# Kernel optimization log

Hardware: AMD Instinct MI355X
Metric: run time of the kernel (lower is better)

Reference implementation:

```python
import jax, jax.numpy as jnp
import numpy as np

LENGTHS = [1024, 768, 896, 512, 1024, 640, 1024, 768, 512, 896, 1024, 704]  # sum = 9792
EMBED, HEADS = 1024, 16
HDIM = EMBED // HEADS  # 64
ROPE_BASE = 10000.0


def _rotate_half(x):
    half = x.shape[-1] // 2
    return jnp.concatenate([-x[..., half:], x[..., :half]], axis=-1)


def setup_inputs() -> dict:
    key = jax.random.key(0)
    ks = jax.random.split(key, 8)
    T = sum(LENGTHS)
    hidden = jax.random.normal(ks[0], (T, EMBED), jnp.float32)
    # RoPE cos/sin: positions restart at 0 within each packed segment
    pos = np.concatenate([np.arange(l) for l in LENGTHS]).astype(np.float32)  # [T]
    inv_freq = 1.0 / (ROPE_BASE ** (np.arange(0, HDIM, 2, dtype=np.float32) / HDIM))
    freqs = np.outer(pos, inv_freq)                       # [T, HDIM//2]
    emb = np.concatenate([freqs, freqs], axis=-1)         # [T, HDIM]
    cos = jnp.asarray(np.cos(emb), jnp.float32)
    sin = jnp.asarray(np.sin(emb), jnp.float32)
    s = 0.02
    q_w = jax.random.normal(ks[1], (EMBED, EMBED), jnp.float32) * s
    k_w = jax.random.normal(ks[2], (EMBED, EMBED), jnp.float32) * s
    v_w = jax.random.normal(ks[3], (EMBED, EMBED), jnp.float32) * s
    out_w = jax.random.normal(ks[4], (EMBED, EMBED), jnp.float32) * s
    q_b = jax.random.normal(ks[5], (EMBED,), jnp.float32) * s
    v_b = jax.random.normal(ks[6], (EMBED,), jnp.float32) * s
    out_b = jax.random.normal(ks[7], (EMBED,), jnp.float32) * s
    return {
        "hidden_states": hidden, "cos": cos, "sin": sin,
        "q_w": q_w, "q_b": q_b, "k_w": k_w, "v_w": v_w, "v_b": v_b,
        "out_w": out_w, "out_b": out_b,
        "seq_len": jnp.array(LENGTHS, jnp.int32),
        "max_seqlen": 1024,
    }


def reference(hidden_states, cos, sin, q_w, q_b, k_w, v_w, v_b, out_w, out_b,
              seq_len, max_seqlen):
    T, D = hidden_states.shape
    H, Dh = HEADS, D // HEADS
    B = seq_len.shape[0]
    L = max_seqlen  # static python int

    # Projections (torch Linear: y = x @ W.T + b; k_proj has no bias)
    q = (hidden_states @ q_w.T + q_b).reshape(T, H, Dh)
    k = (hidden_states @ k_w.T).reshape(T, H, Dh)
    v = (hidden_states @ v_w.T + v_b).reshape(T, H, Dh)

    # Inline RoPE (cos/sin broadcast over heads)
    c = cos[:, None, :]
    s = sin[:, None, :]
    q = q * c + _rotate_half(q) * s
    k = k * c + _rotate_half(k) * s

    # Gather packed tokens into padded [B, L, H, Dh] (honors ragged structure:
    # no [T, T] dense score matrix, only per-segment [L, L] blocks)
    cu = jnp.concatenate([jnp.zeros((1,), seq_len.dtype), jnp.cumsum(seq_len)])[:-1]  # [B] starts
    ar = jnp.arange(L)
    idx = cu[:, None] + ar[None, :]                 # [B, L] token ids
    valid = ar[None, :] < seq_len[:, None]          # [B, L]
    idxc = jnp.minimum(idx, T - 1)
    qp = q[idxc]                                    # [B, L, H, Dh]
    kp = k[idxc]
    vp = v[idxc]

    scale = 1.0 / jnp.sqrt(jnp.float32(Dh))
    scores = jnp.einsum('blhd,bmhd->bhlm', qp, kp) * scale  # [B, H, L, L]
    causal = ar[:, None] >= ar[None, :]             # [L, L]
    mask = valid[:, None, None, :] & causal[None, None, :, :]
    scores = jnp.where(mask, scores, jnp.float32(-1e30))
    probs = jax.nn.softmax(scores, axis=-1)
    attn = jnp.einsum('bhlm,bmhd->blhd', probs, vp).reshape(B, L, D)

    # Scatter valid tokens back to packed layout [T, D]
    attn = attn * valid[..., None].astype(attn.dtype)
    flat = jnp.zeros((T, D), attn.dtype).at[idxc.reshape(-1)].add(attn.reshape(-1, D))
    return flat @ out_w.T + out_b
```

## Files before the change

### kernel.cpp

```cpp
#include <hip/hip_runtime.h>

typedef __bf16 bf16;
typedef __bf16 bf16x8 __attribute__((ext_vector_type(8)));
typedef __bf16 bf16x4 __attribute__((ext_vector_type(4)));
typedef float  f32x4  __attribute__((ext_vector_type(4)));

#define T_TOTAL 9792
#define EMBED   1024
#define NHEAD   16
#define HDIM    64

__constant__ int c_seq_start[12] = {0,1024,1792,2688,3200,4224,4864,5888,6656,7168,8064,9088};
__constant__ int c_tiles_cum[13] = {0,16,28,42,50,66,76,92,104,112,126,142,153};

typedef __attribute__((address_space(1))) unsigned int gu32;
typedef __attribute__((address_space(3))) unsigned int lu32;

__device__ __forceinline__ void load_lds16(const void* g, void* l) {
    __builtin_amdgcn_global_load_lds((gu32*)g, (lu32*)l, 16, 0, 0);
}

__device__ __forceinline__ f32x4 mfma16(bf16x8 a, bf16x8 b, f32x4 c) {
    return __builtin_amdgcn_mfma_f32_16x16x32_bf16(a, b, c, 0, 0, 0);
}

struct CvtArgs {
    const void* src[10];
    bf16*       dst[10];
    int         n[10];
    int         cum[10];
};

__global__ void to_bf16_fused(CvtArgs a, const unsigned short* __restrict__ disc)
{
    const bool f32 = (disc[0] == 0);
    const int blk = blockIdx.x;
    int seg = 0;
    #pragma unroll
    for (int i = 1; i < 10; ++i) if (blk >= a.cum[i]) seg = i;
    int i0 = (blk - a.cum[seg]) * 2048 + threadIdx.x * 8;
    if (i0 >= a.n[seg]) return;
    bf16x8 o;
    if (f32) {
        const float4* s = (const float4*)((const float*)a.src[seg] + i0);
        float4 x = s[0], y = s[1];
        o[0]=(bf16)x.x; o[1]=(bf16)x.y; o[2]=(bf16)x.z; o[3]=(bf16)x.w;
        o[4]=(bf16)y.x; o[5]=(bf16)y.y; o[6]=(bf16)y.z; o[7]=(bf16)y.w;
    } else {
        o = *(const bf16x8*)((const bf16*)a.src[seg] + i0);
    }
    *(bf16x8*)(a.dst[seg] + i0) = o;
}

__device__ __forceinline__ void map_block2(int L, int NX, int NY, int& x, int& y)
{
    const int per = 8 * NY;
    const int nfull = NX >> 3;
    const int full = nfull * per;
    if (L < full) { int sc = L / per, rem = L % per; x = sc * 8 + (rem & 7); y = rem >> 3; }
    else {
        int rem = L - full;
        int tw = NX - nfull * 8;
        x = nfull * 8 + rem % tw; y = rem / tw;
    }
}

__device__ __forceinline__
void gemm_core256(const bf16* __restrict__ A, const bf16* __restrict__ W,
                  int M, int m0, int n0, f32x4 (&acc)[8][4],
                  bf16* lA, bf16* lB)
{
    const int tid  = threadIdx.x;
    const int wave = tid >> 6, lane = tid & 63;
    const int lrow = lane >> 3;
    const int gsw  = (lane & 7) ^ lrow;
    const int ln   = lane & 15, lq = lane >> 4;
    const int e7   = ln & 7;
    const int wm   = (wave >> 2) & 1;
    const int wn   = wave & 3;

    auto stage = [&](int kt, int buf) {
        const int k0 = kt * 64;
        bf16* dA = lA + buf * (256 * 64);
        bf16* dB = lB + buf * (256 * 64);
        #pragma unroll
        for (int j = 0; j < 4; ++j) {
            int r = j * 64 + wave * 8;
            int gr = m0 + r + lrow; if (gr > M - 1) gr = M - 1;
            load_lds16(A + (size_t)gr * EMBED + k0 + gsw * 8, dA + r * 64);
            load_lds16(W + (size_t)(n0 + r + lrow) * EMBED + k0 + gsw * 8, dB + r * 64);
        }
    };

    stage(0, 0);
    __syncthreads();

    for (int kt = 0; kt < 16; ++kt) {
        const int p = kt & 1;
        const bf16* sA = lA + p * (256 * 64);
        const bf16* sB = lB + p * (256 * 64);
        #pragma unroll
        for (int ph = 0; ph < 4; ++ph) {
            const int mh = ph >> 1, nh = ph & 1;
            if (ph == 0 && kt + 1 < 16) stage(kt + 1, p ^ 1);

            bf16x8 af[2][4], bfr[2][2];
            #pragma unroll
            for (int kb = 0; kb < 2; ++kb) {
                #pragma unroll
                for (int mi = 0; mi < 4; ++mi)
                    af[kb][mi] = *(const bf16x8*)
                        &sA[(wm * 128 + mh * 64 + mi * 16 + ln) * 64 + (((kb * 4 + lq) ^ e7) * 8)];
                #pragma unroll
                for (int niq = 0; niq < 2; ++niq)
                    bfr[kb][niq] = *(const bf16x8*)
                        &sB[(wn * 64 + nh * 32 + niq * 16 + ln) * 64 + (((kb * 4 + lq) ^ e7) * 8)];
            }
            __builtin_amdgcn_s_barrier();
            asm volatile("s_waitcnt lgkmcnt(0)" ::: "memory");
            __builtin_amdgcn_s_setprio(1);
            #pragma unroll
            for (int kb = 0; kb < 2; ++kb)
                #pragma unroll
                for (int mi = 0; mi < 4; ++mi)
                    #pragma unroll
                    for (int niq = 0; niq < 2; ++niq)
                        acc[mh * 4 + mi][nh * 2 + niq] =
                            mfma16(af[kb][mi], bfr[kb][niq], acc[mh * 4 + mi][nh * 2 + niq]);
            __builtin_amdgcn_s_setprio(0);
            if (ph == 3 && kt + 1 < 16)
                asm volatile("s_waitcnt vmcnt(0)" ::: "memory");
            __builtin_amdgcn_s_barrier();
        }
    }
}

__global__ __launch_bounds__(512, 2)
void gemm_qkv(const bf16* __restrict__ A,
              const bf16* __restrict__ Wq, const bf16* __restrict__ Wk,
              const bf16* __restrict__ Wv, const bf16* __restrict__ qb,
              const bf16* __restrict__ vb,
              const bf16* __restrict__ cosb, const bf16* __restrict__ sinb,
              bf16* __restrict__ Cq, bf16* __restrict__ Ck,
              bf16* __restrict__ Vt, int M)
{
    __shared__ __align__(16) bf16 lA[2 * 256 * 64];
    __shared__ __align__(16) bf16 lB[2 * 256 * 64];

    int x, yy;
    map_block2(blockIdx.x, 39, 12, x, yy);
    const int which = yy >> 2;
    const int m0 = x * 256, n0 = (yy & 3) * 256;

    const bf16* W = (which == 0) ? Wq : (which == 1) ? Wk : Wv;
    f32x4 acc[8][4] = {};
    gemm_core256(A, W, M, m0, n0, acc, lA, lB);

    const int tid  = threadIdx.x;
    const int wave = tid >> 6, lane = tid & 63;
    const int ln   = lane & 15, lq = lane >> 4;
    const int wm   = (wave >> 2) & 1, wn = wave & 3;
    const int rbase = m0 + wm * 128;
    const int cbase = n0 + wn * 64;

    if (which < 2) {
        bf16* C = (which == 0) ? Cq : Ck;
        const bf16* bias = (which == 0) ? qb : nullptr;
        #pragma unroll
        for (int mi = 0; mi < 8; ++mi) {
            int trow = rbase + mi * 16 + lq * 4;
            if (trow >= M) continue;
            #pragma unroll
            for (int ni = 0; ni < 2; ++ni) {
                int d    = ni * 16 + ln;
                int col0 = cbase + d;
                int col1 = col0 + 32;
                float b0 = bias ? (float)bias[col0] : 0.0f;
                float b1 = bias ? (float)bias[col1] : 0.0f;
                #pragma unroll
                for (int r = 0; r < 4; ++r) {
                    int t = trow + r;
                    float c = (float)cosb[t * HDIM + d];
                    float s = (float)sinb[t * HDIM + d];
                    float x0 = acc[mi][ni][r] + b0;
                    float x1 = acc[mi][ni + 2][r] + b1;
                    C[(size_t)t * EMBED + col0] = (bf16)(x0 * c - x1 * s);
                    C[(size_t)t * EMBED + col1] = (bf16)(x1 * c + x0 * s);
                }
            }
        }
    } else {
        #pragma unroll
        for (int mi = 0; mi < 8; ++mi) {
            int trow = rbase + mi * 16 + lq * 4;
            if (trow >= M) continue;
            #pragma unroll
            for (int ni = 0; ni < 4; ++ni) {
                int d = ni * 16 + ln;
                float bv = (float)vb[cbase + d];
                bf16x4 o;
                #pragma unroll
                for (int r = 0; r < 4; ++r) o[r] = (bf16)(acc[mi][ni][r] + bv);
                *(bf16x4*)&Vt[(size_t)(cbase + d) * T_TOTAL + trow] = o;
            }
        }
    }
}

__global__ __launch_bounds__(512, 2)
void gemm_out(const bf16* __restrict__ A, const bf16* __restrict__ W,
              const bf16* __restrict__ bias, void* __restrict__ out, int M,
              const unsigned short* __restrict__ disc)
{
    __shared__ __align__(16) bf16 lA[2 * 256 * 64];
    __shared__ __align__(16) bf16 lB[2 * 256 * 64];

    int x, yy;
    map_block2(blockIdx.x, 39, 4, x, yy);
    const int m0 = x * 256, n0 = yy * 256;

    f32x4 acc[8][4] = {};
    gemm_core256(A, W, M, m0, n0, acc, lA, lB);

    const bool f32 = (disc[0] == 0);
    const int tid  = threadIdx.x;
    const int wave = tid >> 6, lane = tid & 63;
    const int ln   = lane & 15, lq = lane >> 4;
    const int wm   = (wave >> 2) & 1, wn = wave & 3;
    const int rbase = m0 + wm * 128;
    const int cbase = n0 + wn * 64;

    #pragma unroll
    for (int mi = 0; mi < 8; ++mi) {
        int trow = rbase + mi * 16 + lq * 4;
        if (trow >= M) continue;
        #pragma unroll
        for (int ni = 0; ni < 4; ++ni) {
            int col = cbase + ni * 16 + ln;
            float bv = (float)bias[col];
            #pragma unroll
            for (int r = 0; r < 4; ++r) {
                float v = acc[mi][ni][r] + bv;
                size_t idx = (size_t)(trow + r) * EMBED + col;
                if (f32) ((float*)out)[idx] = v;
                else     ((bf16*)out)[idx]  = (bf16)v;
            }
        }
    }
}

__global__ __launch_bounds__(256, 3)
void attn_kernel(const bf16* __restrict__ Q, const bf16* __restrict__ K,
                 const bf16* __restrict__ Vt, bf16* __restrict__ O)
{
    __shared__ __align__(16) bf16 sK[2][64 * 64];
    __shared__ __align__(16) bf16 sV[2][64 * 64];
    __shared__ __align__(16) bf16 sQP[4 * 16 * 72];

    const int tid  = threadIdx.x;
    const int wave = tid >> 6, lane = tid & 63;
    const int lrow = lane >> 3;
    const int gsw  = (lane & 7) ^ lrow;
    const int ln   = lane & 15, lq = lane >> 4;
    const int e7   = ln & 7;
    const int h = blockIdx.y;

    int b = 0;
    #pragma unroll
    for (int i = 1; i < 13; ++i) if ((int)blockIdx.x >= c_tiles_cum[i]) b = i;
    const int qt = blockIdx.x - c_tiles_cum[b];
    const int t0 = c_seq_start[b] + qt * 64;
    const int kvb0 = c_seq_start[b];

    for (int p = 0; p < 2; ++p) {
        int r = p * 32 + wave * 8;
        load_lds16(Q  + (size_t)(t0 + r + lrow) * EMBED + h * HDIM + gsw * 8, &sQP[r * 64]);
        load_lds16(K  + (size_t)(kvb0 + r + lrow) * EMBED + h * HDIM + gsw * 8, &sK[0][r * 64]);
        load_lds16(Vt + (size_t)(h * HDIM + r + lrow) * T_TOTAL + kvb0 + gsw * 8, &sV[0][r * 64]);
    }

    bf16x8 qf[2];
    f32x4 oacc[4] = {};
    float m_i = -1e30f, l_i = 0.0f;
    const float sc = 0.125f * 1.44269504088896f;
    const int q_loc = wave * 16 + ln;
    bf16* sP = &sQP[wave * 16 * 72];

    for (int j = 0; j <= qt; ++j) {
        __syncthreads();
        const int cur = j & 1;
        if (j == 0) {
            qf[0] = *(const bf16x8*)&sQP[q_loc * 64 + ((0 + lq) ^ e7) * 8];
            qf[1] = *(const bf16x8*)&sQP[q_loc * 64 + ((4 + lq) ^ e7) * 8];
            __syncthreads();
        }
        if (j < qt) {
            const int kvb = kvb0 + (j + 1) * 64;
            const int nxt = cur ^ 1;
            for (int p = 0; p < 2; ++p) {
                int r = p * 32 + wave * 8;
                load_lds16(K  + (size_t)(kvb + r + lrow) * EMBED + h * HDIM + gsw * 8, &sK[nxt][r * 64]);
                load_lds16(Vt + (size_t)(h * HDIM + r + lrow) * T_TOTAL + kvb + gsw * 8, &sV[nxt][r * 64]);
            }
        }

        f32x4 s[4] = {};
        #pragma unroll
        for (int kk = 0; kk < 2; ++kk)
            #pragma unroll
            for (int ni = 0; ni < 4; ++ni) {
                bf16x8 kf = *(const bf16x8*)&sK[cur][(ni * 16 + ln) * 64 + (((kk * 4 + lq) ^ e7) * 8)];
                s[ni] = mfma16(kf, qf[kk], s[ni]);
            }

        float pb[4][4];
        if (j == qt) {
            #pragma unroll
            for (int ni = 0; ni < 4; ++ni)
                #pragma unroll
                for (int r = 0; r < 4; ++r) {
                    int kv = ni * 16 + lq * 4 + r;
                    pb[ni][r] = (kv <= q_loc) ? s[ni][r] * sc : -1e30f;
                }
        } else {
            #pragma unroll
            for (int ni = 0; ni < 4; ++ni)
                #pragma unroll
                for (int r = 0; r < 4; ++r)
                    pb[ni][r] = s[ni][r] * sc;
        }

        float mx = pb[0][0];
        #pragma unroll
        for (int ni = 0; ni < 4; ++ni)
            #pragma unroll
            for (int r = 0; r < 4; ++r) mx = fmaxf(mx, pb[ni][r]);
        mx = fmaxf(mx, __shfl_xor(mx, 16));
        mx = fmaxf(mx, __shfl_xor(mx, 32));
        float mnew  = fmaxf(m_i, mx);
        float alpha = exp2f(m_i - mnew);
        m_i = mnew;

        float rs = 0.0f;
        #pragma unroll
        for (int ni = 0; ni < 4; ++ni)
            #pragma unroll
            for (int r = 0; r < 4; ++r) {
                float pe = exp2f(pb[ni][r] - mnew);
                pb[ni][r] = pe;
                rs += pe;
            }
        rs += __shfl_xor(rs, 16);
        rs += __shfl_xor(rs, 32);
        l_i = l_i * alpha + rs;
        #pragma unroll
        for (int d = 0; d < 4; ++d)
            #pragma unroll
            for (int r = 0; r < 4; ++r) oacc[d][r] *= alpha;

        #pragma unroll
        for (int ni = 0; ni < 4; ++ni) {
            bf16x4 w4;
            #pragma unroll
            for (int r = 0; r < 4; ++r) w4[r] = (bf16)pb[ni][r];
            *(bf16x4*)&sP[ln * 72 + ni * 16 + lq * 4] = w4;
        }
        asm volatile("s_waitcnt lgkmcnt(0)" ::: "memory");

        #pragma unroll
        for (int kk = 0; kk < 2; ++kk) {
            bf16x8 pf = *(const bf16x8*)&sP[ln * 72 + kk * 32 + lq * 8];
            #pragma unroll
            for (int d = 0; d < 4; ++d) {
                bf16x8 vf = *(const bf16x8*)&sV[cur][(d * 16 + ln) * 64 + (((kk * 4 + lq) ^ e7) * 8)];
                oacc[d] = mfma16(vf, pf, oacc[d]);
            }
        }
    }

    const float inv = 1.0f / l_i;
    const size_t row = (size_t)(t0 + q_loc) * EMBED + h * HDIM;
    #pragma unroll
    for (int d = 0; d < 4; ++d) {
        bf16x4 o4;
        #pragma unroll
        for (int r = 0; r < 4; ++r) o4[r] = (bf16)(oacc[d][r] * inv);
        *(bf16x4*)&O[row + d * 16 + lq * 4] = o4;
    }
}

extern "C" void kernel_launch(void* const* d_in, const int* in_sizes, int n_in,
                              void* d_out, int out_size, void* d_ws, size_t ws_size,
                              hipStream_t stream)
{
    const unsigned short* disc = (const unsigned short*)d_in[1];

    const size_t SZ  = (size_t)T_TOTAL * EMBED;
    const size_t CS  = (size_t)T_TOTAL * HDIM;
    const size_t WSZ = (size_t)EMBED * EMBED;

    bf16* p = (bf16*)d_ws;
    bf16* ch   = p; p += SZ;
    bf16* ccos = p; p += CS;
    bf16* csin = p; p += CS;
    bf16* cqw  = p; p += WSZ;
    bf16* ckw  = p; p += WSZ;
    bf16* cvw  = p; p += WSZ;
    bf16* cow  = p; p += WSZ;
    bf16* cqb  = p; p += EMBED;
    bf16* cvb  = p; p += EMBED;
    bf16* cob  = p; p += EMBED;
    bf16* wq   = p; p += SZ;
    bf16* wk   = p; p += SZ;
    bf16* wvt  = p; p += SZ;

    CvtArgs ca;
    const void* srcs[10] = {d_in[0], d_in[1], d_in[2], d_in[3], d_in[5],
                            d_in[6], d_in[8], d_in[4], d_in[7], d_in[9]};
    bf16* dsts[10] = {ch, ccos, csin, cqw, ckw, cvw, cow, cqb, cvb, cob};
    int   ns[10]   = {(int)SZ, (int)CS, (int)CS, (int)WSZ, (int)WSZ,
                      (int)WSZ, (int)WSZ, EMBED, EMBED, EMBED};
    int cum = 0;
    for (int i = 0; i < 10; ++i) {
        ca.src[i] = srcs[i]; ca.dst[i] = dsts[i]; ca.n[i] = ns[i];
        ca.cum[i] = cum;
        cum += (ns[i] + 2047) / 2048;
    }
    to_bf16_fused<<<cum, 256, 0, stream>>>(ca, disc);

    gemm_qkv<<<39 * 12, 512, 0, stream>>>(ch, cqw, ckw, cvw, cqb, cvb,
                                          ccos, csin, wq, wk, wvt, T_TOTAL);
    attn_kernel<<<dim3(153, 16), 256, 0, stream>>>(wq, wk, wvt, wq);
    gemm_out<<<39 * 4, 512, 0, stream>>>(wq, cow, cob, d_out, T_TOTAL, disc);
}
```

Before: 331.4 us.

## Replace GEMM double buffer with a 4-stage K=32 LDS ring pipeline

```diff
diff --git a/kernel.cpp b/kernel.cpp
--- a/kernel.cpp
+++ b/kernel.cpp
@@ -67,71 +67,63 @@
 
 __device__ __forceinline__
 void gemm_core256(const bf16* __restrict__ A, const bf16* __restrict__ W,
-                  int M, int m0, int n0, f32x4 (&acc)[8][4],
-                  bf16* lA, bf16* lB)
+                  int M, int m0, int n0, f32x4 (&acc)[8][4], bf16* lds)
 {
     const int tid  = threadIdx.x;
     const int wave = tid >> 6, lane = tid & 63;
-    const int lrow = lane >> 3;
-    const int gsw  = (lane & 7) ^ lrow;
     const int ln   = lane & 15, lq = lane >> 4;
-    const int e7   = ln & 7;
     const int wm   = (wave >> 2) & 1;
     const int wn   = wave & 3;
 
-    auto stage = [&](int kt, int buf) {
-        const int k0 = kt * 64;
-        bf16* dA = lA + buf * (256 * 64);
-        bf16* dB = lB + buf * (256 * 64);
-        #pragma unroll
-        for (int j = 0; j < 4; ++j) {
-            int r = j * 64 + wave * 8;
-            int gr = m0 + r + lrow; if (gr > M - 1) gr = M - 1;
-            load_lds16(A + (size_t)gr * EMBED + k0 + gsw * 8, dA + r * 64);
-            load_lds16(W + (size_t)(n0 + r + lrow) * EMBED + k0 + gsw * 8, dB + r * 64);
-        }
+    const int srow = tid >> 2;
+    const int sg   = (tid & 3) * 8;
+
+    int r0 = m0 + srow;        if (r0 > M - 1) r0 = M - 1;
+    int r1 = m0 + 128 + srow;  if (r1 > M - 1) r1 = M - 1;
+    const bf16* gA0 = A + (size_t)r0 * EMBED + sg;
+    const bf16* gA1 = A + (size_t)r1 * EMBED + sg;
+    const bf16* gB0 = W + (size_t)(n0 + srow) * EMBED + sg;
+    const bf16* gB1 = W + (size_t)(n0 + 128 + srow) * EMBED + sg;
+
+    auto stage = [&](int t) {
+        const int k0 = t * 32;
+        bf16* dA = lds + (t & 3) * 16384;
+        bf16* dB = dA + 8192;
+        load_lds16(gA0 + k0, dA + tid * 8);
+        load_lds16(gA1 + k0, dA + 4096 + tid * 8);
+        load_lds16(gB0 + k0, dB + tid * 8);
+        load_lds16(gB1 + k0, dB + 4096 + tid * 8);
     };
 
-    stage(0, 0);
-    __syncthreads();
-
-    for (int kt = 0; kt < 16; ++kt) {
-        const int p = kt & 1;
-        const bf16* sA = lA + p * (256 * 64);
-        const bf16* sB = lB + p * (256 * 64);
-        #pragma unroll
-        for (int ph = 0; ph < 4; ++ph) {
-            const int mh = ph >> 1, nh = ph & 1;
-            if (ph == 0 && kt + 1 < 16) stage(kt + 1, p ^ 1);
-
-            bf16x8 af[2][4], bfr[2][2];
-            #pragma unroll
-            for (int kb = 0; kb < 2; ++kb) {
-                #pragma unroll
-                for (int mi = 0; mi < 4; ++mi)
-                    af[kb][mi] = *(const bf16x8*)
-                        &sA[(wm * 128 + mh * 64 + mi * 16 + ln) * 64 + (((kb * 4 + lq) ^ e7) * 8)];
-                #pragma unroll
-                for (int niq = 0; niq < 2; ++niq)
-                    bfr[kb][niq] = *(const bf16x8*)
-                        &sB[(wn * 64 + nh * 32 + niq * 16 + ln) * 64 + (((kb * 4 + lq) ^ e7) * 8)];
-            }
-            __builtin_amdgcn_s_barrier();
-            asm volatile("s_waitcnt lgkmcnt(0)" ::: "memory");
-            __builtin_amdgcn_s_setprio(1);
-            #pragma unroll
-            for (int kb = 0; kb < 2; ++kb)
-                #pragma unroll
-                for (int mi = 0; mi < 4; ++mi)
-                    #pragma unroll
-                    for (int niq = 0; niq < 2; ++niq)
-                        acc[mh * 4 + mi][nh * 2 + niq] =
-                            mfma16(af[kb][mi], bfr[kb][niq], acc[mh * 4 + mi][nh * 2 + niq]);
-            __builtin_amdgcn_s_setprio(0);
-            if (ph == 3 && kt + 1 < 16)
-                asm volatile("s_waitcnt vmcnt(0)" ::: "memory");
-            __builtin_amdgcn_s_barrier();
-        }
+    stage(0); stage(1); stage(2);
+
+    const int aoff = (wm * 128 + ln) * 32 + lq * 8;
+    const int boff = (wn * 64  + ln) * 32 + lq * 8;
+
+    for (int t = 0; t < 32; ++t) {
+        if (t < 30)       asm volatile("s_waitcnt vmcnt(8)" ::: "memory");
+        else if (t == 30) asm volatile("s_waitcnt vmcnt(4)" ::: "memory");
+        else              asm volatile("s_waitcnt vmcnt(0)" ::: "memory");
+        __builtin_amdgcn_s_barrier();
+        if (t + 3 < 32) stage(t + 3);
+
+        const bf16* sA = lds + (t & 3) * 16384;
+        const bf16* sB = sA + 8192;
+        bf16x8 af[8], bfr[4];
+        #pragma unroll
+        for (int mi = 0; mi < 8; ++mi)
+            af[mi] = *(const bf16x8*)&sA[aoff + mi * 512];
+        #pragma unroll
+        for (int ni = 0; ni < 4; ++ni)
+            bfr[ni] = *(const bf16x8*)&sB[boff + ni * 512];
+
+        __builtin_amdgcn_s_setprio(1);
+        #pragma unroll
+        for (int mi = 0; mi < 8; ++mi)
+            #pragma unroll
+            for (int ni = 0; ni < 4; ++ni)
+                acc[mi][ni] = mfma16(af[mi], bfr[ni], acc[mi][ni]);
+        __builtin_amdgcn_s_setprio(0);
     }
 }
 
@@ -144,8 +136,7 @@
               bf16* __restrict__ Cq, bf16* __restrict__ Ck,
               bf16* __restrict__ Vt, int M)
 {
-    __shared__ __align__(16) bf16 lA[2 * 256 * 64];
-    __shared__ __align__(16) bf16 lB[2 * 256 * 64];
+    __shared__ __align__(16) bf16 lds[4 * 16384];
 
     int x, yy;
     map_block2(blockIdx.x, 39, 12, x, yy);
@@ -154,7 +145,7 @@
 
     const bf16* W = (which == 0) ? Wq : (which == 1) ? Wk : Wv;
     f32x4 acc[8][4] = {};
-    gemm_core256(A, W, M, m0, n0, acc, lA, lB);
+    gemm_core256(A, W, M, m0, n0, acc, lds);
 
     const int tid  = threadIdx.x;
     const int wave = tid >> 6, lane = tid & 63;
@@ -212,15 +203,14 @@
               const bf16* __restrict__ bias, void* __restrict__ out, int M,
               const unsigned short* __restrict__ disc)
 {
-    __shared__ __align__(16) bf16 lA[2 * 256 * 64];
-    __shared__ __align__(16) bf16 lB[2 * 256 * 64];
+    __shared__ __align__(16) bf16 lds[4 * 16384];
 
     int x, yy;
     map_block2(blockIdx.x, 39, 4, x, yy);
     const int m0 = x * 256, n0 = yy * 256;
 
     f32x4 acc[8][4] = {};
-    gemm_core256(A, W, M, m0, n0, acc, lA, lB);
+    gemm_core256(A, W, M, m0, n0, acc, lds);
 
     const bool f32 = (disc[0] == 0);
     const int tid  = threadIdx.x;
```

Result: faster. 303.5 us (-8.4%).
